# Optimization experiments

Hardware: AMD Instinct MI355X
Metric: run time of the kernel (lower is better)

## Reference

```python
import jax, jax.numpy as jnp
import numpy as np

N_NODES = 100000
N_EDGES = 1600000
D_FEAT = 64


def setup_inputs() -> dict:
    key = jax.random.key(0)
    k1, k2 = jax.random.split(key)
    x = jax.random.normal(k1, (N_NODES, D_FEAT), dtype=jnp.float32)
    edge_index = jax.random.randint(k2, (2, N_EDGES), 0, N_NODES, dtype=jnp.int64)
    return {"x": x, "edge_index": edge_index}


def reference(x, edge_index):
    # GCNProp (improved=False): remove self loops, add self loops w/ weight 1,
    # symmetric deg^-1/2 normalization, then spmm aggregation.
    N = x.shape[0]
    row, col = edge_index[0], edge_index[1]
    # remove_self_loops: zero the weight of any self-loop edge (math-equivalent
    # to dropping it, and jit-friendly: no data-dependent shapes).
    w = jnp.where(row != col, jnp.ones((), x.dtype), jnp.zeros((), x.dtype))
    # add_self_loops: append N diagonal edges with loop_value = 1 (improved=False)
    loop = jnp.arange(N, dtype=row.dtype)
    row_a = jnp.concatenate([row, loop])          # [E+N]
    col_a = jnp.concatenate([col, loop])          # [E+N]
    w_a = jnp.concatenate([w, jnp.ones((N,), x.dtype)])  # [E+N]
    # degree via scatter_add over rows
    deg = jax.ops.segment_sum(w_a, row_a, num_segments=N)  # [N]
    # deg^-0.5 with inf -> 0
    dinv = jnp.where(deg > 0, jax.lax.rsqrt(deg), jnp.zeros((), x.dtype))
    # edge normalization: deg[row]^-1/2 * w * deg[col]^-1/2
    norm = dinv[row_a] * w_a * dinv[col_a]        # [E+N]
    # spmm: gather neighbor features, scale, scatter-add into rows
    out = jax.ops.segment_sum(norm[:, None] * x[col_a], row_a, num_segments=N)  # [N, D]
    return out
```

## Files before the change

kernel.cpp:

```cpp
#include <hip/hip_runtime.h>

#define N_NODES 100000
#define N_EDGES 1600000
#define D 64
#define NB 391
#define BCAP 4480
#define PBLK 256
#define STPB 1024
#define TPB 512
#define CHUNK ((N_EDGES + PBLK - 1) / PBLK)
#define CURSTRIDE 32
#define CROWS 64

__device__ __forceinline__ unsigned short f2b(float f) {
    unsigned u = __float_as_uint(f);
    u += 0x7FFF + ((u >> 16) & 1);
    return (unsigned short)(u >> 16);
}

__global__ void init_cursor_kernel(int* __restrict__ cursor) {
    int b = blockIdx.x * blockDim.x + threadIdx.x;
    if (b < NB) cursor[b * CURSTRIDE] = b * BCAP;
}

__global__ __launch_bounds__(STPB) void scatter_direct_kernel(const int* __restrict__ ei,
                                                              int* __restrict__ cursor,
                                                              int* __restrict__ epack) {
    __shared__ int h[NB];
    __shared__ int lbase[NB];
    __shared__ int lcur[NB];
    int t = threadIdx.x;
    for (int i = t; i < NB; i += STPB) h[i] = 0;
    __syncthreads();
    int s = blockIdx.x * CHUNK;
    int e = min(s + CHUNK, N_EDGES);
    for (int i = s + t; i < e; i += STPB) {
        int r = ei[i], c = ei[N_EDGES + i];
        if (r != c) atomicAdd(&h[r >> 8], 1);
    }
    __syncthreads();
    for (int i = t; i < NB; i += STPB) {
        int hv = h[i];
        lbase[i] = hv ? atomicAdd(&cursor[i * CURSTRIDE], hv) : 0;
        lcur[i] = 0;
    }
    __syncthreads();
    for (int i = s + t; i < e; i += STPB) {
        int r = ei[i], c = ei[N_EDGES + i];
        if (r != c) {
            int b = r >> 8;
            int p = lbase[b] + atomicAdd(&lcur[b], 1);
            epack[p] = ((r & 255) << 17) | c;
        }
    }
}

__global__ __launch_bounds__(TPB) void csr_sort_kernel(const int* __restrict__ cursor,
                                                       int* __restrict__ epack,
                                                       int2* __restrict__ rowinfo,
                                                       float* __restrict__ dinv) {
    __shared__ int ebuf[BCAP];
    __shared__ int h[256];
    __shared__ int sc[256];
    __shared__ int cur[256];
    int b = blockIdx.x;
    int t = threadIdx.x;
    int base = b * BCAP;
    int n = min(cursor[b * CURSTRIDE] - base, BCAP);
    const int4* ep4 = (const int4*)(epack + base);
    int n4 = n >> 2;
    for (int i = t; i < n4; i += TPB) ((int4*)ebuf)[i] = ep4[i];
    for (int i = (n4 << 2) + t; i < n; i += TPB) ebuf[i] = epack[base + i];
    if (t < 256) h[t] = 0;
    __syncthreads();
    for (int i = t; i < n; i += TPB) atomicAdd(&h[ebuf[i] >> 17], 1);
    __syncthreads();
    int v = 0;
    if (t < 256) { v = h[t]; sc[t] = v; }
    __syncthreads();
    for (int off = 1; off < 256; off <<= 1) {
        int u = (t < 256 && t >= off) ? sc[t - off] : 0;
        __syncthreads();
        if (t < 256) sc[t] += u;
        __syncthreads();
    }
    if (t < 256) {
        int excl = sc[t] - v;
        int row = b * 256 + t;
        if (row < N_NODES) {
            rowinfo[row] = make_int2(base + excl, v);
            dinv[row] = rsqrtf((float)(1 + v));
        }
        cur[t] = excl;
    }
    __syncthreads();
    for (int i = t; i < n; i += TPB) {
        int p = ebuf[i];
        int pos = atomicAdd(&cur[p >> 17], 1);
        epack[base + pos] = (p & 0x1FFFF) << 7;
    }
}

__global__ __launch_bounds__(256) void convert_kernel(const float* __restrict__ x,
                                                      const float* __restrict__ dinv,
                                                      unsigned short* __restrict__ xs) {
    __shared__ float dv[CROWS];
    int b = blockIdx.x;
    int t = threadIdx.x;
    int r0 = b * CROWS;
    int nrows = min(CROWS, N_NODES - r0);
    if (t < nrows) dv[t] = dinv[r0 + t];
    __syncthreads();
    const float4* x4 = (const float4*)x;
    ushort4* xs4 = (ushort4*)xs;
    for (int i = t; i < nrows * 16; i += 256) {
        int rl = i >> 4;
        float4 vv = x4[(size_t)(r0 + rl) * 16 + (i & 15)];
        float dd = dv[rl];
        ushort4 o;
        o.x = f2b(vv.x * dd);
        o.y = f2b(vv.y * dd);
        o.z = f2b(vv.z * dd);
        o.w = f2b(vv.w * dd);
        xs4[(size_t)(r0 + rl) * 16 + (i & 15)] = o;
    }
}

__global__ __launch_bounds__(256) void gather_kernel(const unsigned short* __restrict__ xs,
                                                     const int2* __restrict__ rowinfo,
                                                     const int* __restrict__ colidx,
                                                     float* __restrict__ out) {
    int t = blockIdx.x * blockDim.x + threadIdx.x;
    int r = t >> 6;
    int lane = t & 63;
    if (r >= N_NODES) return;
    int lp = lane & 31;
    int hf = lane >> 5;
    int lpo = lp << 2;
    int2 ri = rowinfo[r];
    int start = ri.x;
    int end = start + ri.y;
    float dr = rsqrtf((float)(1 + ri.y));
    const char* xsb = (const char*)xs;
    float ax = 0.0f, ay = 0.0f;
    if (hf == 0) {
        unsigned v = *(const unsigned*)(xsb + (((size_t)r) << 7) + lpo);
        ax = __uint_as_float(v << 16);
        ay = __uint_as_float(v & 0xFFFF0000u);
    }
    for (int j = start; j < end; j += 64) {
        int idx = j + lane;
        int cj = (idx < end) ? colidx[idx] : 0;
        int n = min(64, end - j);
        int k = 0;
        for (; 2 * (k + 8) <= n; k += 8) {
            int s0 = __shfl(cj, 2 * k + hf);
            int s1 = __shfl(cj, 2 * k + 2 + hf);
            int s2 = __shfl(cj, 2 * k + 4 + hf);
            int s3 = __shfl(cj, 2 * k + 6 + hf);
            int s4 = __shfl(cj, 2 * k + 8 + hf);
            int s5 = __shfl(cj, 2 * k + 10 + hf);
            int s6 = __shfl(cj, 2 * k + 12 + hf);
            int s7 = __shfl(cj, 2 * k + 14 + hf);
            unsigned v0 = *(const unsigned*)(xsb + (unsigned)(s0 + lpo));
            unsigned v1 = *(const unsigned*)(xsb + (unsigned)(s1 + lpo));
            unsigned v2 = *(const unsigned*)(xsb + (unsigned)(s2 + lpo));
            unsigned v3 = *(const unsigned*)(xsb + (unsigned)(s3 + lpo));
            unsigned v4 = *(const unsigned*)(xsb + (unsigned)(s4 + lpo));
            unsigned v5 = *(const unsigned*)(xsb + (unsigned)(s5 + lpo));
            unsigned v6 = *(const unsigned*)(xsb + (unsigned)(s6 + lpo));
            unsigned v7 = *(const unsigned*)(xsb + (unsigned)(s7 + lpo));
            float a0 = __uint_as_float(v0 << 16), b0 = __uint_as_float(v0 & 0xFFFF0000u);
            float a1 = __uint_as_float(v1 << 16), b1 = __uint_as_float(v1 & 0xFFFF0000u);
            float a2 = __uint_as_float(v2 << 16), b2 = __uint_as_float(v2 & 0xFFFF0000u);
            float a3 = __uint_as_float(v3 << 16), b3 = __uint_as_float(v3 & 0xFFFF0000u);
            float a4 = __uint_as_float(v4 << 16), b4 = __uint_as_float(v4 & 0xFFFF0000u);
            float a5 = __uint_as_float(v5 << 16), b5 = __uint_as_float(v5 & 0xFFFF0000u);
            float a6 = __uint_as_float(v6 << 16), b6 = __uint_as_float(v6 & 0xFFFF0000u);
            float a7 = __uint_as_float(v7 << 16), b7 = __uint_as_float(v7 & 0xFFFF0000u);
            ax += ((a0 + a1) + (a2 + a3)) + ((a4 + a5) + (a6 + a7));
            ay += ((b0 + b1) + (b2 + b3)) + ((b4 + b5) + (b6 + b7));
        }
        for (; 2 * (k + 4) <= n; k += 4) {
            int s0 = __shfl(cj, 2 * k + hf);
            int s1 = __shfl(cj, 2 * k + 2 + hf);
            int s2 = __shfl(cj, 2 * k + 4 + hf);
            int s3 = __shfl(cj, 2 * k + 6 + hf);
            unsigned v0 = *(const unsigned*)(xsb + (unsigned)(s0 + lpo));
            unsigned v1 = *(const unsigned*)(xsb + (unsigned)(s1 + lpo));
            unsigned v2 = *(const unsigned*)(xsb + (unsigned)(s2 + lpo));
            unsigned v3 = *(const unsigned*)(xsb + (unsigned)(s3 + lpo));
            float a0 = __uint_as_float(v0 << 16), b0 = __uint_as_float(v0 & 0xFFFF0000u);
            float a1 = __uint_as_float(v1 << 16), b1 = __uint_as_float(v1 & 0xFFFF0000u);
            float a2 = __uint_as_float(v2 << 16), b2 = __uint_as_float(v2 & 0xFFFF0000u);
            float a3 = __uint_as_float(v3 << 16), b3 = __uint_as_float(v3 & 0xFFFF0000u);
            ax += (a0 + a1) + (a2 + a3);
            ay += (b0 + b1) + (b2 + b3);
        }
        for (; 2 * k < n; k++) {
            int src = 2 * k + hf;
            int s0 = __shfl(cj, (src < n) ? src : (n - 1));
            unsigned v0 = *(const unsigned*)(xsb + (unsigned)(s0 + lpo));
            if (src < n) {
                ax += __uint_as_float(v0 << 16);
                ay += __uint_as_float(v0 & 0xFFFF0000u);
            }
        }
    }
    ax += __shfl_xor(ax, 32);
    ay += __shfl_xor(ay, 32);
    if (hf == 0) {
        float2 o;
        o.x = dr * ax;
        o.y = dr * ay;
        ((float2*)out)[(size_t)r * 32 + lp] = o;
    }
}

extern "C" void kernel_launch(void* const* d_in, const int* in_sizes, int n_in,
                              void* d_out, int out_size, void* d_ws, size_t ws_size,
                              hipStream_t stream) {
    const float* x = (const float*)d_in[0];
    const int* ei = (const int*)d_in[1];
    float* out = (float*)d_out;

    int* cursor = (int*)d_ws;
    int2* rowinfo = (int2*)(cursor + NB * CURSTRIDE);
    float* dinv = (float*)(rowinfo + N_NODES);
    int* epack = (int*)(dinv + N_NODES);
    unsigned short* xs = (unsigned short*)(epack + NB * BCAP);

    init_cursor_kernel<<<(NB + 255) / 256, 256, 0, stream>>>(cursor);
    scatter_direct_kernel<<<PBLK, STPB, 0, stream>>>(ei, cursor, epack);
    csr_sort_kernel<<<NB, TPB, 0, stream>>>(cursor, epack, rowinfo, dinv);
    convert_kernel<<<(N_NODES + CROWS - 1) / CROWS, 256, 0, stream>>>(x, dinv, xs);
    gather_kernel<<<(N_NODES * D + 255) / 256, 256, 0, stream>>>(xs, rowinfo, epack, out);
}
```

Baseline: 153.5 us.

## Unroll edge scatter, fuse histogram into load, wave-scan, nontemporal memory ops

The edge scatter now loads all of a thread's edges into registers in one unrolled pass instead of reading edge_index twice. The CSR sort builds its histogram while copying edges into shared memory and replaces the barrier-heavy LDS scan with a wavefront shuffle scan. The cursor init kernel becomes a memset, with the bucket base added at use. Nontemporal loads and stores are applied across kernels to reduce cache pollution, which may instead hurt reuse where data is read again.

```diff
diff --git a/kernel.cpp b/kernel.cpp
--- a/kernel.cpp
+++ b/kernel.cpp
@@ -9,18 +9,19 @@
 #define STPB 1024
 #define TPB 512
 #define CHUNK ((N_EDGES + PBLK - 1) / PBLK)
+#define K_FULL (CHUNK / STPB)
+#define K_REM (CHUNK - K_FULL * STPB)
 #define CURSTRIDE 32
 #define CROWS 64
+
+typedef int iv4 __attribute__((ext_vector_type(4)));
+typedef float fv4 __attribute__((ext_vector_type(4)));
+typedef float fv2 __attribute__((ext_vector_type(2)));
 
 __device__ __forceinline__ unsigned short f2b(float f) {
     unsigned u = __float_as_uint(f);
     u += 0x7FFF + ((u >> 16) & 1);
     return (unsigned short)(u >> 16);
-}
-
-__global__ void init_cursor_kernel(int* __restrict__ cursor) {
-    int b = blockIdx.x * blockDim.x + threadIdx.x;
-    if (b < NB) cursor[b * CURSTRIDE] = b * BCAP;
 }
 
 __global__ __launch_bounds__(STPB) void scatter_direct_kernel(const int* __restrict__ ei,
@@ -32,27 +33,52 @@
     int t = threadIdx.x;
     for (int i = t; i < NB; i += STPB) h[i] = 0;
     __syncthreads();
-    int s = blockIdx.x * CHUNK;
-    int e = min(s + CHUNK, N_EDGES);
-    for (int i = s + t; i < e; i += STPB) {
-        int r = ei[i], c = ei[N_EDGES + i];
-        if (r != c) atomicAdd(&h[r >> 8], 1);
-    }
+    int s = blockIdx.x * CHUNK + t;
+    int r0 = __builtin_nontemporal_load(ei + s);
+    int c0 = __builtin_nontemporal_load(ei + N_EDGES + s);
+    int r1 = __builtin_nontemporal_load(ei + s + 1 * STPB);
+    int c1 = __builtin_nontemporal_load(ei + N_EDGES + s + 1 * STPB);
+    int r2 = __builtin_nontemporal_load(ei + s + 2 * STPB);
+    int c2 = __builtin_nontemporal_load(ei + N_EDGES + s + 2 * STPB);
+    int r3 = __builtin_nontemporal_load(ei + s + 3 * STPB);
+    int c3 = __builtin_nontemporal_load(ei + N_EDGES + s + 3 * STPB);
+    int r4 = __builtin_nontemporal_load(ei + s + 4 * STPB);
+    int c4 = __builtin_nontemporal_load(ei + N_EDGES + s + 4 * STPB);
+    int r5 = __builtin_nontemporal_load(ei + s + 5 * STPB);
+    int c5 = __builtin_nontemporal_load(ei + N_EDGES + s + 5 * STPB);
+    int r6 = 0, c6 = 0;
+    if (t < K_REM) {
+        r6 = __builtin_nontemporal_load(ei + s + 6 * STPB);
+        c6 = __builtin_nontemporal_load(ei + N_EDGES + s + 6 * STPB);
+    }
+    if (r0 != c0) atomicAdd(&h[r0 >> 8], 1);
+    if (r1 != c1) atomicAdd(&h[r1 >> 8], 1);
+    if (r2 != c2) atomicAdd(&h[r2 >> 8], 1);
+    if (r3 != c3) atomicAdd(&h[r3 >> 8], 1);
+    if (r4 != c4) atomicAdd(&h[r4 >> 8], 1);
+    if (r5 != c5) atomicAdd(&h[r5 >> 8], 1);
+    if (r6 != c6) atomicAdd(&h[r6 >> 8], 1);
     __syncthreads();
     for (int i = t; i < NB; i += STPB) {
         int hv = h[i];
-        lbase[i] = hv ? atomicAdd(&cursor[i * CURSTRIDE], hv) : 0;
+        lbase[i] = hv ? (i * BCAP + atomicAdd(&cursor[i * CURSTRIDE], hv)) : 0;
         lcur[i] = 0;
     }
     __syncthreads();
-    for (int i = s + t; i < e; i += STPB) {
-        int r = ei[i], c = ei[N_EDGES + i];
-        if (r != c) {
-            int b = r >> 8;
-            int p = lbase[b] + atomicAdd(&lcur[b], 1);
-            epack[p] = ((r & 255) << 17) | c;
-        }
-    }
+#define PUT_EDGE(rr, cc)                                            \
+    if (rr != cc) {                                                 \
+        int bb = rr >> 8;                                           \
+        int p = lbase[bb] + atomicAdd(&lcur[bb], 1);                \
+        epack[p] = ((rr & 255) << 17) | cc;                         \
+    }
+    PUT_EDGE(r0, c0)
+    PUT_EDGE(r1, c1)
+    PUT_EDGE(r2, c2)
+    PUT_EDGE(r3, c3)
+    PUT_EDGE(r4, c4)
+    PUT_EDGE(r5, c5)
+    PUT_EDGE(r6, c6)
+#undef PUT_EDGE
 }
 
 __global__ __launch_bounds__(TPB) void csr_sort_kernel(const int* __restrict__ cursor,
@@ -61,35 +87,51 @@
                                                        float* __restrict__ dinv) {
     __shared__ int ebuf[BCAP];
     __shared__ int h[256];
-    __shared__ int sc[256];
     __shared__ int cur[256];
+    __shared__ int wtot[4];
     int b = blockIdx.x;
     int t = threadIdx.x;
     int base = b * BCAP;
-    int n = min(cursor[b * CURSTRIDE] - base, BCAP);
-    const int4* ep4 = (const int4*)(epack + base);
+    int n = min(cursor[b * CURSTRIDE], BCAP);
+    if (t < 256) h[t] = 0;
+    __syncthreads();
+    const iv4* ep4 = (const iv4*)(epack + base);
     int n4 = n >> 2;
-    for (int i = t; i < n4; i += TPB) ((int4*)ebuf)[i] = ep4[i];
-    for (int i = (n4 << 2) + t; i < n; i += TPB) ebuf[i] = epack[base + i];
-    if (t < 256) h[t] = 0;
-    __syncthreads();
-    for (int i = t; i < n; i += TPB) atomicAdd(&h[ebuf[i] >> 17], 1);
-    __syncthreads();
-    int v = 0;
-    if (t < 256) { v = h[t]; sc[t] = v; }
-    __syncthreads();
-    for (int off = 1; off < 256; off <<= 1) {
-        int u = (t < 256 && t >= off) ? sc[t - off] : 0;
-        __syncthreads();
-        if (t < 256) sc[t] += u;
-        __syncthreads();
-    }
+    for (int i = t; i < n4; i += TPB) {
+        iv4 v = __builtin_nontemporal_load(ep4 + i);
+        ((iv4*)ebuf)[i] = v;
+        atomicAdd(&h[v.x >> 17], 1);
+        atomicAdd(&h[v.y >> 17], 1);
+        atomicAdd(&h[v.z >> 17], 1);
+        atomicAdd(&h[v.w >> 17], 1);
+    }
+    for (int i = (n4 << 2) + t; i < n; i += TPB) {
+        int v = epack[base + i];
+        ebuf[i] = v;
+        atomicAdd(&h[v >> 17], 1);
+    }
+    __syncthreads();
+    int lane = t & 63;
+    int w = t >> 6;
+    int myh = (t < 256) ? h[t] : 0;
+    int v = myh;
+    for (int off = 1; off < 64; off <<= 1) {
+        int u = __shfl_up(v, off);
+        if (lane >= off) v += u;
+    }
+    if (t < 256 && lane == 63) wtot[w] = v;
+    __syncthreads();
     if (t < 256) {
-        int excl = sc[t] - v;
+        int woff = 0;
+        if (w > 0) woff += wtot[0];
+        if (w > 1) woff += wtot[1];
+        if (w > 2) woff += wtot[2];
+        int incl = v + woff;
+        int excl = incl - myh;
         int row = b * 256 + t;
         if (row < N_NODES) {
-            rowinfo[row] = make_int2(base + excl, v);
-            dinv[row] = rsqrtf((float)(1 + v));
+            rowinfo[row] = make_int2(base + excl, myh);
+            dinv[row] = rsqrtf((float)(1 + myh));
         }
         cur[t] = excl;
     }
@@ -111,11 +153,11 @@
     int nrows = min(CROWS, N_NODES - r0);
     if (t < nrows) dv[t] = dinv[r0 + t];
     __syncthreads();
-    const float4* x4 = (const float4*)x;
+    const fv4* x4 = (const fv4*)x;
     ushort4* xs4 = (ushort4*)xs;
     for (int i = t; i < nrows * 16; i += 256) {
         int rl = i >> 4;
-        float4 vv = x4[(size_t)(r0 + rl) * 16 + (i & 15)];
+        fv4 vv = __builtin_nontemporal_load(x4 + (size_t)(r0 + rl) * 16 + (i & 15));
         float dd = dv[rl];
         ushort4 o;
         o.x = f2b(vv.x * dd);
@@ -150,7 +192,7 @@
     }
     for (int j = start; j < end; j += 64) {
         int idx = j + lane;
-        int cj = (idx < end) ? colidx[idx] : 0;
+        int cj = (idx < end) ? __builtin_nontemporal_load(colidx + idx) : 0;
         int n = min(64, end - j);
         int k = 0;
         for (; 2 * (k + 8) <= n; k += 8) {
@@ -210,10 +252,10 @@
     ax += __shfl_xor(ax, 32);
     ay += __shfl_xor(ay, 32);
     if (hf == 0) {
-        float2 o;
+        fv2 o;
         o.x = dr * ax;
         o.y = dr * ay;
-        ((float2*)out)[(size_t)r * 32 + lp] = o;
+        __builtin_nontemporal_store(o, (fv2*)out + (size_t)r * 32 + lp);
     }
 }
 
@@ -230,7 +272,7 @@
     int* epack = (int*)(dinv + N_NODES);
     unsigned short* xs = (unsigned short*)(epack + NB * BCAP);
 
-    init_cursor_kernel<<<(NB + 255) / 256, 256, 0, stream>>>(cursor);
+    (void)hipMemsetAsync(cursor, 0, NB * CURSTRIDE * sizeof(int), stream);
     scatter_direct_kernel<<<PBLK, STPB, 0, stream>>>(ei, cursor, epack);
     csr_sort_kernel<<<NB, TPB, 0, stream>>>(cursor, epack, rowinfo, dinv);
     convert_kernel<<<(N_NODES + CROWS - 1) / CROWS, 256, 0, stream>>>(x, dinv, xs);
```

New measurement: 156.2 us. Within noise of the previous version (+1.8%).
